# Kernel optimization log

Hardware: AMD Instinct MI355X
Metric: run time of the kernel (lower is better)

## Reference

```python
import jax, jax.numpy as jnp
import numpy as np
from jax import lax

B, T, D = 4, 4096, 1024
H, d = 4, 64
EPS = 1e-6

def pos_unit(x):
    # positive feature map (elu+1) normalized to unit L2 norm along feature dim
    p = jax.nn.elu(x) + 1.0
    return p / (jnp.linalg.norm(p, axis=-1, keepdims=True) + EPS)

def setup_inputs() -> dict:
    key = jax.random.key(0)
    ks = jax.random.split(key, 5)
    s_in = 1.0 / np.sqrt(D)
    s_hd = 1.0 / np.sqrt(H * d)
    return {
        "x": jax.random.normal(ks[0], (B, T, D), dtype=jnp.float32),
        "Wq": jax.random.normal(ks[1], (H * d, D), dtype=jnp.float32) * s_in,
        "Wk": jax.random.normal(ks[2], (H * d, D), dtype=jnp.float32) * s_in,
        "Wv": jax.random.normal(ks[3], (H * d, D), dtype=jnp.float32) * s_in,
        "Wo": jax.random.normal(ks[4], (D, H * d), dtype=jnp.float32) * s_hd,
    }

def reference(x, Wq, Wk, Wv, Wo):
    Bx, Tx, Dx = x.shape
    q = (x @ Wq.T).reshape(Bx, Tx, H, d)
    k = (x @ Wk.T).reshape(Bx, Tx, H, d)
    v = (x @ Wv.T).reshape(Bx, Tx, H, d)
    q = pos_unit(q)
    k = pos_unit(k)
    # time-major for scan: [T, B, H, d]
    qT = jnp.transpose(q, (1, 0, 2, 3))
    kT = jnp.transpose(k, (1, 0, 2, 3))
    vT = jnp.transpose(v, (1, 0, 2, 3))
    kv0 = jnp.zeros((Bx, H, d, d), dtype=x.dtype)  # [B,H,j,d]
    kc0 = jnp.zeros((Bx, H, d), dtype=x.dtype)

    def step(carry, inp):
        kv_cum, k_cum = carry
        qt, kt, vt = inp  # each [B,H,d]
        kv_cum = kv_cum + jnp.einsum('bhd,bhj->bhjd', kt, vt)
        k_cum = k_cum + kt
        num = jnp.einsum('bhd,bhjd->bhj', qt, kv_cum)
        den = jnp.einsum('bhd,bhd->bh', qt, k_cum)[..., None] + EPS
        return (kv_cum, k_cum), num / den

    (kv_f, kc_f), yT = lax.scan(step, (kv0, kc0), (qT, kT, vT))
    y = jnp.transpose(yT, (1, 0, 2, 3)).reshape(Bx, Tx, H * d)
    y = y @ Wo.T
    return y, kv_f, kc_f
```

## Files before the change

### kernel.cpp

```cpp
#include <hip/hip_runtime.h>
#include <hip/hip_bf16.h>
#include <math.h>

#define T_SEQ   4096
#define NB      4
#define NH      4
#define DH      64
#define DM      1024
#define MR      16384
#define NQKV    768
#define CH      64
#define NCH     64
#define SST     4160
#define BHN     16

typedef __attribute__((ext_vector_type(4))) float          f32x4;
typedef __attribute__((ext_vector_type(8))) short          s16x8;
typedef __attribute__((ext_vector_type(4))) unsigned short u16x4;

__device__ __forceinline__ float bf2f(unsigned short u) {
  union { unsigned int i; float f; } c; c.i = ((unsigned int)u) << 16; return c.f;
}
__device__ __forceinline__ unsigned short f2bf(float f) {
  union { float f; unsigned int i; } c; c.f = f;
  unsigned int i = c.i;
  return (unsigned short)((i + 0x7fffu + ((i >> 16) & 1u)) >> 16);
}
__device__ __forceinline__ s16x8 pack8(f32x4 lo, f32x4 hi) {
  s16x8 r;
  r[0] = (short)f2bf(lo.x); r[1] = (short)f2bf(lo.y);
  r[2] = (short)f2bf(lo.z); r[3] = (short)f2bf(lo.w);
  r[4] = (short)f2bf(hi.x); r[5] = (short)f2bf(hi.y);
  r[6] = (short)f2bf(hi.z); r[7] = (short)f2bf(hi.w);
  return r;
}
__device__ __forceinline__ void gl_lds16(const unsigned short* g, unsigned short* l) {
  __builtin_amdgcn_global_load_lds(
      (const __attribute__((address_space(1))) unsigned int*)g,
      (__attribute__((address_space(3))) unsigned int*)l, 16, 0, 0);
}

__global__ __launch_bounds__(256) void convert_kernel(
    const float* __restrict__ X,
    const float* __restrict__ Wq, const float* __restrict__ Wk,
    const float* __restrict__ Wv,
    unsigned short* __restrict__ Xb, unsigned short* __restrict__ Wb)
{
  const long long NX = 16777216LL;
  const long long NW = 786432LL;
  const long long total = NX + NW;
  const long long stride = (long long)gridDim.x * 256 * 8;
  for (long long i = ((long long)blockIdx.x * 256 + threadIdx.x) * 8;
       i < total; i += stride) {
    const float* src;
    unsigned short* dst;
    if (i < NX) { src = X + i; dst = Xb + i; }
    else {
      const long long e = i - NX;
      const int w = (int)(e >> 18);
      const long long rr = e & 262143LL;
      src = (w == 0 ? Wq : w == 1 ? Wk : Wv) + rr;
      dst = Wb + e;
    }
    const f32x4 lo = *(const f32x4*)src;
    const f32x4 hi = *(const f32x4*)(src + 4);
    *(s16x8*)dst = pack8(lo, hi);
  }
}

__global__ __launch_bounds__(256, 2) void gemm_qkv_kernel(
    const unsigned short* __restrict__ Xb,
    const unsigned short* __restrict__ Wb,
    unsigned short* __restrict__ C)
{
  constexpr int K = DM;
  constexpr int N = NQKV;
  __shared__ __align__(16) unsigned short sA[128 * 32];
  __shared__ __align__(16) unsigned short sB[128 * 32];

  const int tid  = threadIdx.x;
  const int wave = tid >> 6;
  const int lane = tid & 63;
  const int quad = lane >> 4;
  const int l16  = lane & 15;
  const int wm = (wave >> 1) * 64;
  const int wn = (wave & 1) * 64;

  const int row0 = blockIdx.x * 128;
  const int bn   = blockIdx.y;
  const int srow = tid >> 2;
  const int scol = ((tid & 3) ^ (srow & 3)) * 8;
  const unsigned short* Ag = Xb + (size_t)(row0     + srow) * K + scol;
  const unsigned short* Bg = Wb + (size_t)(bn * 128 + srow) * K + scol;
  unsigned short* sAp = sA + tid * 8;
  unsigned short* sBp = sB + tid * 8;

  const int ra = (quad ^ (l16 & 3)) * 8;

  f32x4 acc[4][4];
  #pragma unroll
  for (int i = 0; i < 4; i++)
    #pragma unroll
    for (int j = 0; j < 4; j++) acc[i][j] = (f32x4){0.f, 0.f, 0.f, 0.f};

  for (int kt = 0; kt < K; kt += 32) {
    __syncthreads();
    gl_lds16(Ag + kt,                  sAp);
    gl_lds16(Ag + kt + (size_t)64 * K, sAp + 2048);
    gl_lds16(Bg + kt,                  sBp);
    gl_lds16(Bg + kt + (size_t)64 * K, sBp + 2048);
    __syncthreads();
    s16x8 af[4], bw[4];
    #pragma unroll
    for (int i = 0; i < 4; i++)
      af[i] = *(const s16x8*)(sA + (wm + i * 16 + l16) * 32 + ra);
    #pragma unroll
    for (int j = 0; j < 4; j++)
      bw[j] = *(const s16x8*)(sB + (wn + j * 16 + l16) * 32 + ra);
    #pragma unroll
    for (int i = 0; i < 4; i++)
      #pragma unroll
      for (int j = 0; j < 4; j++)
        acc[i][j] = __builtin_amdgcn_mfma_f32_16x16x32_bf16(af[i], bw[j], acc[i][j], 0, 0, 0);
  }

  const int colb = bn * 128 + wn;
  #pragma unroll
  for (int i = 0; i < 4; i++) {
    const int r = row0 + wm + i * 16 + quad * 4;
    #pragma unroll
    for (int j = 0; j < 4; j++) {
      const int cc = colb + j * 16 + l16;
      #pragma unroll
      for (int g = 0; g < 4; g++)
        C[(size_t)(r + g) * N + cc] = f2bf(acc[i][j][g]);
    }
  }
}

__global__ __launch_bounds__(256, 2) void gemm_out_kernel(
    const unsigned short* __restrict__ Y,
    const float* __restrict__ Wo,
    float* __restrict__ Out)
{
  constexpr int K = 256;
  constexpr int N = DM;
  __shared__ unsigned short sA[128 * 32];
  __shared__ unsigned short sB[128 * 32];

  const int tid  = threadIdx.x;
  const int wave = tid >> 6;
  const int lane = tid & 63;
  const int quad = lane >> 4;
  const int l16  = lane & 15;
  const int wm = (wave >> 1) * 64;
  const int wn = (wave & 1) * 64;

  const int row0  = blockIdx.x * 128;
  const int bcol0 = blockIdx.y * 128;

  const int srow = tid >> 2;
  const int scol = ((tid & 3) ^ (srow & 3)) * 8;
  const unsigned short* Ag = Y  + (size_t)(row0  + srow) * K + scol;
  const float*          Bg = Wo + (size_t)(bcol0 + srow) * K + scol;
  unsigned short* sAp = sA + tid * 8;
  unsigned short* sBp = sB + tid * 8;

  const int ra = (quad ^ (l16 & 3)) * 8;

  f32x4 acc[4][4];
  #pragma unroll
  for (int i = 0; i < 4; i++)
    #pragma unroll
    for (int j = 0; j < 4; j++) acc[i][j] = (f32x4){0.f, 0.f, 0.f, 0.f};

  for (int kt = 0; kt < K; kt += 32) {
    const s16x8 a0 = *(const s16x8*)(Ag + kt);
    const s16x8 a1 = *(const s16x8*)(Ag + kt + (size_t)64 * K);
    const f32x4 b0l = *(const f32x4*)(Bg + kt);
    const f32x4 b0h = *(const f32x4*)(Bg + kt + 4);
    const f32x4 b1l = *(const f32x4*)(Bg + kt + (size_t)64 * K);
    const f32x4 b1h = *(const f32x4*)(Bg + kt + (size_t)64 * K + 4);
    __syncthreads();
    *(s16x8*)sAp          = a0;
    *(s16x8*)(sAp + 2048) = a1;
    *(s16x8*)sBp          = pack8(b0l, b0h);
    *(s16x8*)(sBp + 2048) = pack8(b1l, b1h);
    __syncthreads();
    s16x8 af[4], bw[4];
    #pragma unroll
    for (int i = 0; i < 4; i++)
      af[i] = *(const s16x8*)(sA + (wm + i * 16 + l16) * 32 + ra);
    #pragma unroll
    for (int j = 0; j < 4; j++)
      bw[j] = *(const s16x8*)(sB + (wn + j * 16 + l16) * 32 + ra);
    #pragma unroll
    for (int i = 0; i < 4; i++)
      #pragma unroll
      for (int j = 0; j < 4; j++)
        acc[i][j] = __builtin_amdgcn_mfma_f32_16x16x32_bf16(af[i], bw[j], acc[i][j], 0, 0, 0);
  }

  #pragma unroll
  for (int i = 0; i < 4; i++) {
    const int r = row0 + wm + i * 16 + quad * 4;
    #pragma unroll
    for (int j = 0; j < 4; j++) {
      const int cc = bcol0 + wn + j * 16 + l16;
      #pragma unroll
      for (int g = 0; g < 4; g++)
        Out[(size_t)(r + g) * N + cc] = acc[i][j][g];
    }
  }
}

__global__ __launch_bounds__(256) void chunk_sums_kernel(
    const unsigned short* __restrict__ qkv,
    float* __restrict__ cs)
{
  const int blk = blockIdx.x;
  const int bh = blk >> 6, c = blk & 63;
  const int b = bh >> 2, h = bh & 3;
  __shared__ __align__(16) unsigned short sKt[64 * 64];
  __shared__ __align__(16) unsigned short sVt[64 * 64];
  __shared__ float sPart[4 * 64];
  const int wave = threadIdx.x >> 6, lane = threadIdx.x & 63;
  const int quad = lane >> 4, l16 = lane & 15;
  const size_t rowbase = ((size_t)b * T_SEQ + (size_t)c * CH) * NQKV + h * DH;

  float kacc = 0.f;
  #pragma unroll 4
  for (int tt = 0; tt < 16; tt++) {
    const int t = tt * 4 + wave;
    const unsigned short* r = qkv + rowbase + (size_t)t * NQKV;
    const float kx = bf2f(r[256 + lane]);
    const unsigned short vu = r[512 + lane];
    float pk = kx > 0.f ? kx + 1.f : __expf(kx);
    float sk = pk * pk;
    #pragma unroll
    for (int o = 32; o > 0; o >>= 1) sk += __shfl_xor(sk, o, 64);
    const float kn = pk / (sqrtf(sk) + 1e-6f);
    kacc += kn;
    const int sw = (lane & 7) << 3;
    sKt[lane * 64 + (t ^ sw)] = f2bf(kn);
    sVt[lane * 64 + (t ^ sw)] = vu;
  }
  sPart[wave * 64 + lane] = kacc;
  __syncthreads();

  const int wr = (wave >> 1) * 32;
  const int wc = (wave & 1) * 32;
  f32x4 acc[2][2];
  #pragma unroll
  for (int i = 0; i < 2; i++)
    #pragma unroll
    for (int j = 0; j < 2; j++) acc[i][j] = (f32x4){0.f, 0.f, 0.f, 0.f};

  #pragma unroll
  for (int ks = 0; ks < 2; ks++) {
    const int grp = ks * 4 + quad;
    s16x8 ak[2], bv[2];
    #pragma unroll
    for (int i = 0; i < 2; i++) {
      const int rk = wr + i * 16 + l16;
      ak[i] = *(const s16x8*)(sKt + rk * 64 + ((grp ^ (rk & 7)) << 3));
    }
    #pragma unroll
    for (int j = 0; j < 2; j++) {
      const int rj = wc + j * 16 + l16;
      bv[j] = *(const s16x8*)(sVt + rj * 64 + ((grp ^ (rj & 7)) << 3));
    }
    #pragma unroll
    for (int i = 0; i < 2; i++)
      #pragma unroll
      for (int j = 0; j < 2; j++)
        acc[i][j] = __builtin_amdgcn_mfma_f32_16x16x32_bf16(ak[i], bv[j], acc[i][j], 0, 0, 0);
  }

  float* o = cs + (size_t)blk * SST;
  #pragma unroll
  for (int i = 0; i < 2; i++)
    #pragma unroll
    for (int j = 0; j < 2; j++)
      #pragma unroll
      for (int g = 0; g < 4; g++) {
        const int dd = wr + i * 16 + quad * 4 + g;
        const int jj = wc + j * 16 + l16;
        o[dd * 64 + jj] = acc[i][j][g];
      }
  if (threadIdx.x < 64)
    o[4096 + threadIdx.x] = sPart[threadIdx.x] + sPart[64 + threadIdx.x]
                          + sPart[128 + threadIdx.x] + sPart[192 + threadIdx.x];
}

__global__ __launch_bounds__(256) void scan_kernel(
    float* __restrict__ cs, float* __restrict__ outTail)
{
  const int gid = blockIdx.x * 256 + threadIdx.x;
  const int bh = gid / SST;
  const int e  = gid - bh * SST;
  float run = 0.f;
  size_t idx = (size_t)bh * NCH * SST + e;
  for (int c = 0; c < NCH; c++, idx += SST) {
    const float v = cs[idx];
    cs[idx] = run;
    run += v;
  }
  if (e < 4096) {
    const int dd = e >> 6, j = e & 63;
    outTail[(size_t)bh * 4096 + j * 64 + dd] = run;
  } else {
    const int dd = e - 4096;
    outTail[BHN * 4096 + (size_t)bh * 64 + dd] = run;
  }
}

__global__ __launch_bounds__(256, 4) void chunk_out_kernel(
    const unsigned short* __restrict__ qkv,
    const float* __restrict__ st,
    unsigned short* __restrict__ yatt)
{
  const int blk = blockIdx.x;
  const int bh = blk >> 6;
  const int c  = blk & 63;
  const int b = bh >> 2, h = bh & 3;

  __shared__ __align__(16) unsigned short sQ [64 * 64];
  __shared__ __align__(16) unsigned short sKA[64 * 64];
  __shared__ __align__(16) unsigned short sVt[64 * 64];
  __shared__ __align__(16) unsigned short sSt[64 * 64];
  __shared__ float sKc[64];
  __shared__ float sDen[64];

  const int tid  = threadIdx.x;
  const int wave = tid >> 6, lane = tid & 63;
  const int quad = lane >> 4, l16 = lane & 15;
  const size_t rowbase = ((size_t)b * T_SEQ + (size_t)c * CH) * NQKV + h * DH;

  #pragma unroll 4
  for (int tt = 0; tt < 16; tt++) {
    const int t = tt * 4 + wave;
    const unsigned short* r = qkv + rowbase + (size_t)t * NQKV;
    const float qx = bf2f(r[lane]);
    const float kx = bf2f(r[256 + lane]);
    const unsigned short vu = r[512 + lane];
    float pq = qx > 0.f ? qx + 1.f : __expf(qx);
    float pk = kx > 0.f ? kx + 1.f : __expf(kx);
    float sq = pq * pq, sk = pk * pk;
    #pragma unroll
    for (int o = 32; o > 0; o >>= 1) {
      sq += __shfl_xor(sq, o, 64);
      sk += __shfl_xor(sk, o, 64);
    }
    const int sw = (t & 7) << 3;
    sQ [t * 64 + (lane ^ sw)] = f2bf(pq / (sqrtf(sq) + 1e-6f));
    sKA[t * 64 + (lane ^ sw)] = f2bf(pk / (sqrtf(sk) + 1e-6f));
    sVt[lane * 64 + (t ^ ((lane & 7) << 3))] = vu;
  }
  const float* stp = st + (size_t)blk * SST;
  for (int i = tid; i < 1024; i += 256) {
    const f32x4 s4 = ((const f32x4*)stp)[i];
    const int d = i >> 4, j0 = (i & 15) << 2;
    #pragma unroll
    for (int g = 0; g < 4; g++) {
      const int j = j0 + g;
      sSt[j * 64 + (d ^ ((j & 7) << 3))] = f2bf(s4[g]);
    }
  }
  if (tid < 64) sKc[tid] = stp[4096 + tid];
  __syncthreads();

  const int wr = (wave >> 1) * 32;
  const int wc = (wave & 1) * 32;

  f32x4 accA[2][2];
  #pragma unroll
  for (int i = 0; i < 2; i++)
    #pragma unroll
    for (int j = 0; j < 2; j++) accA[i][j] = (f32x4){0.f, 0.f, 0.f, 0.f};

  #pragma unroll
  for (int ks = 0; ks < 2; ks++) {
    const int grp = ks * 4 + quad;
    s16x8 aq[2], bk[2];
    #pragma unroll
    for (int i = 0; i < 2; i++) {
      const int rq = wr + i * 16 + l16;
      aq[i] = *(const s16x8*)(sQ + rq * 64 + ((grp ^ (rq & 7)) << 3));
    }
    #pragma unroll
    for (int j = 0; j < 2; j++) {
      const int rk = wc + j * 16 + l16;
      bk[j] = *(const s16x8*)(sKA + rk * 64 + ((grp ^ (rk & 7)) << 3));
    }
    #pragma unroll
    for (int i = 0; i < 2; i++)
      #pragma unroll
      for (int j = 0; j < 2; j++)
        accA[i][j] = __builtin_amdgcn_mfma_f32_16x16x32_bf16(aq[i], bk[j], accA[i][j], 0, 0, 0);
  }
  __syncthreads();

  #pragma unroll
  for (int i = 0; i < 2; i++)
    #pragma unroll
    for (int j = 0; j < 2; j++)
      #pragma unroll
      for (int g = 0; g < 4; g++) {
        const int t = wr + i * 16 + quad * 4 + g;
        const int s = wc + j * 16 + l16;
        const float av = (s <= t) ? accA[i][j][g] : 0.f;
        sKA[t * 64 + (s ^ ((t & 7) << 3))] = f2bf(av);
      }
  __syncthreads();

  {
    const int t = tid >> 2, p = tid & 3;
    const int sw = (t & 7) << 3;
    float s = 0.f;
    #pragma unroll
    for (int e = 0; e < 16; e++) {
      const int d = p * 16 + e;
      s += bf2f(sKA[t * 64 + d]);
      s += bf2f(sQ[t * 64 + (d ^ sw)]) * sKc[d];
    }
    s += __shfl_xor(s, 1, 64);
    s += __shfl_xor(s, 2, 64);
    if (p == 0) sDen[t] = s + 1e-6f;
  }
  __syncthreads();

  f32x4 acc[2][2];
  #pragma unroll
  for (int i = 0; i < 2; i++)
    #pragma unroll
    for (int j = 0; j < 2; j++) acc[i][j] = (f32x4){0.f, 0.f, 0.f, 0.f};

  #pragma unroll
  for (int ks = 0; ks < 2; ks++) {
    const int grp = ks * 4 + quad;
    s16x8 aq[2], bs[2];
    #pragma unroll
    for (int i = 0; i < 2; i++) {
      const int rq = wr + i * 16 + l16;
      aq[i] = *(const s16x8*)(sQ + rq * 64 + ((grp ^ (rq & 7)) << 3));
    }
    #pragma unroll
    for (int j = 0; j < 2; j++) {
      const int rj = wc + j * 16 + l16;
      bs[j] = *(const s16x8*)(sSt + rj * 64 + ((grp ^ (rj & 7)) << 3));
    }
    #pragma unroll
    for (int i = 0; i < 2; i++)
      #pragma unroll
      for (int j = 0; j < 2; j++)
        acc[i][j] = __builtin_amdgcn_mfma_f32_16x16x32_bf16(aq[i], bs[j], acc[i][j], 0, 0, 0);
  }
  #pragma unroll
  for (int ks = 0; ks < 2; ks++) {
    const int grp = ks * 4 + quad;
    s16x8 aa[2], bv[2];
    #pragma unroll
    for (int i = 0; i < 2; i++) {
      const int rt = wr + i * 16 + l16;
      aa[i] = *(const s16x8*)(sKA + rt * 64 + ((grp ^ (rt & 7)) << 3));
    }
    #pragma unroll
    for (int j = 0; j < 2; j++) {
      const int rj = wc + j * 16 + l16;
      bv[j] = *(const s16x8*)(sVt + rj * 64 + ((grp ^ (rj & 7)) << 3));
    }
    #pragma unroll
    for (int i = 0; i < 2; i++)
      #pragma unroll
      for (int j = 0; j < 2; j++)
        acc[i][j] = __builtin_amdgcn_mfma_f32_16x16x32_bf16(aa[i], bv[j], acc[i][j], 0, 0, 0);
  }

  #pragma unroll
  for (int i = 0; i < 2; i++)
    #pragma unroll
    for (int g = 0; g < 4; g++) {
      const int t = wr + i * 16 + quad * 4 + g;
      const float inv = 1.f / sDen[t];
      #pragma unroll
      for (int j = 0; j < 2; j++) {
        const int jj = wc + j * 16 + l16;
        const size_t o = ((size_t)b * T_SEQ + (size_t)c * CH + t) * 256 + h * 64 + jj;
        yatt[o] = f2bf(acc[i][j][g] * inv);
      }
    }
}

extern "C" void kernel_launch(void* const* d_in, const int* in_sizes, int n_in,
                              void* d_out, int out_size, void* d_ws, size_t ws_size,
                              hipStream_t stream) {
  const float* X  = (const float*)d_in[0];
  const float* Wq = (const float*)d_in[1];
  const float* Wk = (const float*)d_in[2];
  const float* Wv = (const float*)d_in[3];
  const float* Wo = (const float*)d_in[4];
  float* out = (float*)d_out;

  unsigned short* qkvb = (unsigned short*)d_out;
  unsigned short* Xb   = (unsigned short*)((char*)d_out + 25165824ull);
  unsigned short* Wb   = Xb + 16777216;
  float* outTail = out + 16777216;
  float*          cs   = (float*)d_ws;
  unsigned short* yatt = (unsigned short*)((char*)d_ws + 17039360ull);

  convert_kernel   <<<4096,         256, 0, stream>>>(X, Wq, Wk, Wv, Xb, Wb);
  gemm_qkv_kernel  <<<dim3(128, 6), 256, 0, stream>>>(Xb, Wb, qkvb);
  chunk_sums_kernel<<<BHN * NCH,    256, 0, stream>>>(qkvb, cs);
  scan_kernel      <<<(BHN * SST) / 256, 256, 0, stream>>>(cs, outTail);
  chunk_out_kernel <<<BHN * NCH,    256, 0, stream>>>(qkvb, cs, yatt);
  gemm_out_kernel  <<<dim3(128, 8), 256, 0, stream>>>(yatt, Wo, out);
}
```

Before: 210.7 us.

## Fuse elu+1 and L2 normalization of q/k into QKV GEMM epilogue

Applies the positive feature map and per-head unit normalization to q and k inside the QKV projection epilogue, using a 16-lane shuffle reduction across each 64-column head. The downstream chunk-state and output kernels then read pre-normalized q/k directly and drop their per-row exp, shuffle and sqrt work, with the output kernel loading q/k tiles straight into LDS through async global-to-LDS copies. The output GEMM's A operand load also switches to the direct-to-LDS path. Normalized values are now rounded to bf16 once at the GEMM store, and q/k are no longer kept unnormalized anywhere.

```diff
diff --git a/kernel.cpp b/kernel.cpp
--- a/kernel.cpp
+++ b/kernel.cpp
@@ -125,15 +125,41 @@
   }
 
   const int colb = bn * 128 + wn;
-  #pragma unroll
-  for (int i = 0; i < 4; i++) {
-    const int r = row0 + wm + i * 16 + quad * 4;
-    #pragma unroll
-    for (int j = 0; j < 4; j++) {
-      const int cc = colb + j * 16 + l16;
-      #pragma unroll
-      for (int g = 0; g < 4; g++)
-        C[(size_t)(r + g) * N + cc] = f2bf(acc[i][j][g]);
+  if (bn < 4) {
+    #pragma unroll
+    for (int i = 0; i < 4; i++) {
+      const int r = row0 + wm + i * 16 + quad * 4;
+      #pragma unroll
+      for (int g = 0; g < 4; g++) {
+        float p[4];
+        float ss = 0.f;
+        #pragma unroll
+        for (int j = 0; j < 4; j++) {
+          const float a = acc[i][j][g];
+          p[j] = a > 0.f ? a + 1.f : __expf(a);
+          ss += p[j] * p[j];
+        }
+        ss += __shfl_xor(ss, 1, 64);
+        ss += __shfl_xor(ss, 2, 64);
+        ss += __shfl_xor(ss, 4, 64);
+        ss += __shfl_xor(ss, 8, 64);
+        const float inv = 1.f / (sqrtf(ss) + 1e-6f);
+        #pragma unroll
+        for (int j = 0; j < 4; j++)
+          C[(size_t)(r + g) * N + colb + j * 16 + l16] = f2bf(p[j] * inv);
+      }
+    }
+  } else {
+    #pragma unroll
+    for (int i = 0; i < 4; i++) {
+      const int r = row0 + wm + i * 16 + quad * 4;
+      #pragma unroll
+      for (int j = 0; j < 4; j++) {
+        const int cc = colb + j * 16 + l16;
+        #pragma unroll
+        for (int g = 0; g < 4; g++)
+          C[(size_t)(r + g) * N + cc] = f2bf(acc[i][j][g]);
+      }
     }
   }
 }
@@ -145,8 +171,8 @@
 {
   constexpr int K = 256;
   constexpr int N = DM;
-  __shared__ unsigned short sA[128 * 32];
-  __shared__ unsigned short sB[128 * 32];
+  __shared__ __align__(16) unsigned short sA[128 * 32];
+  __shared__ __align__(16) unsigned short sB[128 * 32];
 
   const int tid  = threadIdx.x;
   const int wave = tid >> 6;
@@ -175,15 +201,13 @@
     for (int j = 0; j < 4; j++) acc[i][j] = (f32x4){0.f, 0.f, 0.f, 0.f};
 
   for (int kt = 0; kt < K; kt += 32) {
-    const s16x8 a0 = *(const s16x8*)(Ag + kt);
-    const s16x8 a1 = *(const s16x8*)(Ag + kt + (size_t)64 * K);
     const f32x4 b0l = *(const f32x4*)(Bg + kt);
     const f32x4 b0h = *(const f32x4*)(Bg + kt + 4);
     const f32x4 b1l = *(const f32x4*)(Bg + kt + (size_t)64 * K);
     const f32x4 b1h = *(const f32x4*)(Bg + kt + (size_t)64 * K + 4);
     __syncthreads();
-    *(s16x8*)sAp          = a0;
-    *(s16x8*)(sAp + 2048) = a1;
+    gl_lds16(Ag + kt,                  sAp);
+    gl_lds16(Ag + kt + (size_t)64 * K, sAp + 2048);
     *(s16x8*)sBp          = pack8(b0l, b0h);
     *(s16x8*)(sBp + 2048) = pack8(b1l, b1h);
     __syncthreads();
@@ -233,16 +257,11 @@
   for (int tt = 0; tt < 16; tt++) {
     const int t = tt * 4 + wave;
     const unsigned short* r = qkv + rowbase + (size_t)t * NQKV;
-    const float kx = bf2f(r[256 + lane]);
+    const unsigned short ku = r[256 + lane];
     const unsigned short vu = r[512 + lane];
-    float pk = kx > 0.f ? kx + 1.f : __expf(kx);
-    float sk = pk * pk;
-    #pragma unroll
-    for (int o = 32; o > 0; o >>= 1) sk += __shfl_xor(sk, o, 64);
-    const float kn = pk / (sqrtf(sk) + 1e-6f);
-    kacc += kn;
+    kacc += bf2f(ku);
     const int sw = (lane & 7) << 3;
-    sKt[lane * 64 + (t ^ sw)] = f2bf(kn);
+    sKt[lane * 64 + (t ^ sw)] = ku;
     sVt[lane * 64 + (t ^ sw)] = vu;
   }
   sPart[wave * 64 + lane] = kacc;
@@ -337,25 +356,21 @@
   const int quad = lane >> 4, l16 = lane & 15;
   const size_t rowbase = ((size_t)b * T_SEQ + (size_t)c * CH) * NQKV + h * DH;
 
+  #pragma unroll
+  for (int p = 0; p < 2; p++) {
+    const int e  = p * 2048 + tid * 8;
+    const int t  = e >> 6;
+    const int c0 = e & 56;
+    const int sc = c0 ^ ((t & 7) << 3);
+    const unsigned short* src = qkv + rowbase + (size_t)t * NQKV + sc;
+    gl_lds16(src,       sQ  + e);
+    gl_lds16(src + 256, sKA + e);
+  }
   #pragma unroll 4
   for (int tt = 0; tt < 16; tt++) {
     const int t = tt * 4 + wave;
-    const unsigned short* r = qkv + rowbase + (size_t)t * NQKV;
-    const float qx = bf2f(r[lane]);
-    const float kx = bf2f(r[256 + lane]);
-    const unsigned short vu = r[512 + lane];
-    float pq = qx > 0.f ? qx + 1.f : __expf(qx);
-    float pk = kx > 0.f ? kx + 1.f : __expf(kx);
-    float sq = pq * pq, sk = pk * pk;
-    #pragma unroll
-    for (int o = 32; o > 0; o >>= 1) {
-      sq += __shfl_xor(sq, o, 64);
-      sk += __shfl_xor(sk, o, 64);
-    }
-    const int sw = (t & 7) << 3;
-    sQ [t * 64 + (lane ^ sw)] = f2bf(pq / (sqrtf(sq) + 1e-6f));
-    sKA[t * 64 + (lane ^ sw)] = f2bf(pk / (sqrtf(sk) + 1e-6f));
-    sVt[lane * 64 + (t ^ ((lane & 7) << 3))] = vu;
+    sVt[lane * 64 + (t ^ ((lane & 7) << 3))] =
+        qkv[rowbase + (size_t)t * NQKV + 512 + lane];
   }
   const float* stp = st + (size_t)blk * SST;
   for (int i = tid; i < 1024; i += 256) {
```

Measured after the change: 199.3 us. 1.06x faster.
